# Kernel optimization log

Hardware: AMD Instinct MI355X
Metric: run time of the kernel (lower is better)

Reference implementation:

```python
import jax, jax.numpy as jnp
import numpy as np

BATCH = 4096          # batch_size from init
TEMP = 0.1            # temperature
EPS = 1e-8            # torch CosineSimilarity eps
N = 2 * BATCH


def _neg_flat_idx(bs):
    """Static flat indices of the negative entries of the (N,N) sim matrix:
    everything except the main diagonal and the +-bs diagonals (positives)."""
    n = 2 * bs
    mask = np.ones((n, n), dtype=bool)
    np.fill_diagonal(mask, False)
    r = np.arange(bs)
    mask[r, bs + r] = False
    mask[bs + r, r] = False
    return np.nonzero(mask.reshape(-1))[0]


NEG_IDX = jnp.asarray(_neg_flat_idx(BATCH))  # (N*(N-2),)


def setup_inputs() -> dict:
    key = jax.random.key(0)
    k1, k2 = jax.random.split(key)
    msg = jax.random.normal(k1, (N, 512), dtype=jnp.float32)
    img = jax.random.normal(k2, (N, 512), dtype=jnp.float32)
    return {"msg": msg, "img": img}


def reference(msg, img):
    # cosine similarity via normalized GEMM (norms clamped at eps, per torch)
    mn = msg / jnp.maximum(jnp.linalg.norm(msg, axis=1, keepdims=True), EPS)
    im = img / jnp.maximum(jnp.linalg.norm(img, axis=1, keepdims=True), EPS)
    sim = jnp.matmul(mn, im.T) / TEMP                      # (N, N)

    sim_i_j = jnp.diagonal(sim, offset=BATCH)              # (BATCH,)
    sim_j_i = jnp.diagonal(sim, offset=-BATCH)             # (BATCH,)
    positives = jnp.concatenate([sim_i_j, sim_j_i])[:, None]   # (N, 1)
    negatives = sim.reshape(-1)[NEG_IDX].reshape(N, N - 2)     # (N, N-2)

    logits = jnp.concatenate([positives, negatives], axis=1)   # (N, N-1)
    logp = jax.nn.log_softmax(logits, axis=1)
    # labels are all zero; CrossEntropyLoss(reduction='sum') / N
    loss = -jnp.sum(logp[:, 0]) / N
    acc = jnp.mean((jnp.argmax(logits, axis=1) == 0).astype(jnp.float32))
    return loss, acc
```

## Files before the change

### kernel.cpp

```cpp
#include <hip/hip_runtime.h>
#include <hip/hip_bf16.h>


#define NROWS 8192
#define BATCHD 4096
#define DIM 512
#define BM 128
#define BN 128
#define BK 32
#define NSTEP (DIM / BK)
#define SHIFT 10.0f

typedef short bf16x8 __attribute__((ext_vector_type(8)));
typedef float f32x4 __attribute__((ext_vector_type(4)));

#define GLDS(g, l)                                                             \
    __builtin_amdgcn_global_load_lds(                                          \
        (const __attribute__((address_space(1))) void*)(g),                    \
        (__attribute__((address_space(3))) void*)(l), 16, 0, 0)

__device__ __forceinline__ unsigned f2u_ord(float f) {
    unsigned u = __float_as_uint(f);
    return (u & 0x80000000u) ? ~u : (u | 0x80000000u);
}
__device__ __forceinline__ float u2f_ord(unsigned e) {
    return (e & 0x80000000u) ? __uint_as_float(e & 0x7fffffffu) : __uint_as_float(~e);
}
__device__ __forceinline__ short f2bf(float f) {
    unsigned u = __float_as_uint(f);
    return (short)((u + 0x7fffu + ((u >> 16) & 1u)) >> 16);
}

__global__ __launch_bounds__(64) void normalize_bf16_both(const float* __restrict__ msg,
                                                          const float* __restrict__ img,
                                                          short* __restrict__ mnb,
                                                          short* __restrict__ imb,
                                                          float* __restrict__ rowsum,
                                                          unsigned* __restrict__ rowmax,
                                                          float* __restrict__ accum) {
    if (blockIdx.x < 128) {
        const int i = blockIdx.x * 64 + threadIdx.x;
        rowsum[i] = 0.f;
        rowmax[i] = 0u;
        if (i < 2) accum[i] = 0.f;
    }
    int row = blockIdx.x;
    const float* in;
    short* out;
    float scale;
    if (row < NROWS) { in = msg; out = mnb; scale = 10.0f; }
    else { row -= NROWS; in = img; out = imb; scale = 1.0f; }
    const int lane = threadIdx.x;
    const float* src = in + (size_t)row * DIM + lane * 8;
    float4 v0 = *(const float4*)(src);
    float4 v1 = *(const float4*)(src + 4);
    float ss = v0.x*v0.x + v0.y*v0.y + v0.z*v0.z + v0.w*v0.w
             + v1.x*v1.x + v1.y*v1.y + v1.z*v1.z + v1.w*v1.w;
    #pragma unroll
    for (int off = 1; off < 64; off <<= 1) ss += __shfl_xor(ss, off);
    const float inv = scale / fmaxf(sqrtf(ss), 1e-8f);
    float vv[8] = {v0.x, v0.y, v0.z, v0.w, v1.x, v1.y, v1.z, v1.w};
    bf16x8 o;
    #pragma unroll
    for (int j = 0; j < 8; ++j) o[j] = f2bf(vv[j] * inv);
    *(bf16x8*)(out + (size_t)row * DIM + lane * 8) = o;
}

__global__ __launch_bounds__(256, 4) void simloss_mfma(const short* __restrict__ A,
                                                       const short* __restrict__ B,
                                                       float* __restrict__ rowsum,
                                                       unsigned* __restrict__ rowmax,
                                                       float* __restrict__ rowpos) {
    __shared__ short As[2][BM * BK];
    __shared__ short Bs[2][BN * BK];

    const int tid = threadIdx.x;
    const int lane = tid & 63;
    const int g = lane >> 4;
    const int r16 = lane & 15;
    const int wid = tid >> 6;
    const int wr = wid >> 1;
    const int wc = wid & 1;

    const int bid = blockIdx.x;
    const int xcd = bid & 7;
    const int l = bid >> 3;
    const int by = xcd * 8 + (l & 7);
    const int bx = l >> 3;
    const int rowBase = by * BM;
    const int colBase = bx * BN;

    const int s0 = tid, s1 = tid + 256;
    const int r0 = s0 >> 2, r1 = s1 >> 2;
    const int c0 = (s0 & 3) ^ ((r0 >> 1) & 3);
    const int c1 = (s1 & 3) ^ ((r1 >> 1) & 3);
    const short* gA0 = A + (size_t)(rowBase + r0) * DIM + c0 * 8;
    const short* gA1 = A + (size_t)(rowBase + r1) * DIM + c1 * 8;
    const short* gB0 = B + (size_t)(colBase + r0) * DIM + c0 * 8;
    const short* gB1 = B + (size_t)(colBase + r1) * DIM + c1 * 8;

#define STAGE(b, koff)                                  \
    do {                                                \
        GLDS(gA0 + (koff), &As[b][tid * 8]);            \
        GLDS(gA1 + (koff), &As[b][2048 + tid * 8]);     \
        GLDS(gB0 + (koff), &Bs[b][tid * 8]);            \
        GLDS(gB1 + (koff), &Bs[b][2048 + tid * 8]);     \
    } while (0)

    const int swz = (r16 >> 1) & 3;
    const int aBase = (wr * 64 + r16) * BK + ((g ^ swz) * 8);
    const int bBase = (wc * 64 + r16) * BK + ((g ^ swz) * 8);

    f32x4 acc[4][4] = {};

#define VMCNT(n) asm volatile("s_waitcnt vmcnt(" #n ")" ::: "memory")
#define BAR() __builtin_amdgcn_s_barrier()

    STAGE(0, 0);

    for (int t = 0; t < NSTEP; ++t) {
        const int b = t & 1;
        if (t < NSTEP - 1) {
            STAGE(b ^ 1, (t + 1) * BK);
            VMCNT(4);
        } else {
            VMCNT(0);
        }
        BAR();
        bf16x8 af[4], bfr[4];
        #pragma unroll
        for (int m = 0; m < 4; ++m)
            af[m] = *(const bf16x8*)&As[b][aBase + m * 16 * BK];
        #pragma unroll
        for (int n = 0; n < 4; ++n)
            bfr[n] = *(const bf16x8*)&Bs[b][bBase + n * 16 * BK];
        __builtin_amdgcn_s_setprio(1);
        #pragma unroll
        for (int m = 0; m < 4; ++m)
            #pragma unroll
            for (int n = 0; n < 4; ++n)
                acc[m][n] = __builtin_amdgcn_mfma_f32_16x16x32_bf16(
                    af[m], bfr[n], acc[m][n], 0, 0, 0);
        __builtin_amdgcn_s_setprio(0);
        BAR();
    }

    __syncthreads();
    float* ssum = (float*)&As[0][0];
    float* smx = ssum + 256;
    const int baseRow = rowBase + wr * 64 + g * 4;
    const int baseCol = colBase + wc * 64 + r16;
    #pragma unroll
    for (int m = 0; m < 4; ++m) {
        #pragma unroll
        for (int reg = 0; reg < 4; ++reg) {
            const int i = baseRow + m * 16 + reg;
            const int partner = i ^ BATCHD;
            float sum = 0.f, mx = -1e30f;
            #pragma unroll
            for (int n = 0; n < 4; ++n) {
                const int j = baseCol + n * 16;
                const float s = acc[m][n][reg];
                const bool isDiag = (j == i);
                const bool isPos = (j == partner);
                float e = __expf(s - SHIFT);
                if (isDiag) e = 0.f;
                sum += e;
                if (!isDiag && !isPos) mx = fmaxf(mx, s);
                if (isPos) rowpos[i] = s;
            }
            #pragma unroll
            for (int off = 1; off < 16; off <<= 1) {
                sum += __shfl_xor(sum, off);
                mx = fmaxf(mx, __shfl_xor(mx, off));
            }
            if (r16 == 0) {
                const int rloc = wr * 64 + m * 16 + g * 4 + reg;
                ssum[rloc * 2 + wc] = sum;
                smx[rloc * 2 + wc] = mx;
            }
        }
    }
    __syncthreads();
    if (tid < BM) {
        const float s = ssum[tid * 2 + 0] + ssum[tid * 2 + 1];
        const float mx = fmaxf(smx[tid * 2 + 0], smx[tid * 2 + 1]);
        const int i = rowBase + tid;
        atomicAdd(&rowsum[i], s);
        atomicMax(&rowmax[i], f2u_ord(mx));
    }
#undef STAGE
#undef VMCNT
#undef BAR
}

__global__ __launch_bounds__(256) void finalize_partial(const float* __restrict__ rowsum,
                                                        const unsigned* __restrict__ rowmax,
                                                        const float* __restrict__ rowpos,
                                                        float* __restrict__ accum) {
    const int tid = threadIdx.x;
    const int i = blockIdx.x * 256 + tid;
    const float lse = SHIFT + logf(rowsum[i]);
    const float pos = rowpos[i];
    float lossAcc = lse - pos;
    float hitAcc = (pos >= u2f_ord(rowmax[i])) ? 1.f : 0.f;
    __shared__ float sl[256], sa[256];
    sl[tid] = lossAcc; sa[tid] = hitAcc;
    __syncthreads();
    for (int s = 128; s > 0; s >>= 1) {
        if (tid < s) { sl[tid] += sl[tid + s]; sa[tid] += sa[tid + s]; }
        __syncthreads();
    }
    if (tid == 0) {
        atomicAdd(&accum[0], sl[0]);
        atomicAdd(&accum[1], sa[0]);
    }
}

__global__ void finalize_write(const float* __restrict__ accum, float* __restrict__ out) {
    if (threadIdx.x == 0) {
        out[0] = accum[0] / (float)NROWS;
        out[1] = accum[1] / (float)NROWS;
    }
}

extern "C" void kernel_launch(void* const* d_in, const int* in_sizes, int n_in,
                              void* d_out, int out_size, void* d_ws, size_t ws_size,
                              hipStream_t stream) {
    const float* msg = (const float*)d_in[0];
    const float* img = (const float*)d_in[1];
    float* out = (float*)d_out;

    char* ws = (char*)d_ws;
    const size_t matBytes = (size_t)NROWS * DIM * sizeof(short);
    short* mnb = (short*)ws;
    short* imb = (short*)(ws + matBytes);
    float* rowsum = (float*)(ws + 2 * matBytes);
    unsigned* rowmax = (unsigned*)(ws + 2 * matBytes + NROWS * sizeof(float));
    float* rowpos = (float*)(ws + 2 * matBytes + 2 * NROWS * sizeof(float));
    float* accum = (float*)(ws + 2 * matBytes + 3 * NROWS * sizeof(float));

    normalize_bf16_both<<<2 * NROWS, 64, 0, stream>>>(msg, img, mnb, imb,
                                                      rowsum, rowmax, accum);

    simloss_mfma<<<(NROWS / BM) * (NROWS / BN), 256, 0, stream>>>(mnb, imb, rowsum,
                                                                  rowmax, rowpos);

    finalize_partial<<<NROWS / 256, 256, 0, stream>>>(rowsum, rowmax, rowpos, accum);
    finalize_write<<<1, 64, 0, stream>>>(accum, out);
}
```

Before: 105.7 us.

## Load A fragments directly from global into registers, bypassing LDS

The A operand is no longer staged through shared memory. Each wave loads its A fragments straight from global memory into registers, double-buffered across k-steps with the next step prefetched, while B keeps its LDS double buffer. This cuts LDS footprint and LDS traffic for A and removes the A shared-memory reads. In exchange, A rows shared by the two wave columns are now loaded twice from global/L2, and the loads are uncoalesced 16-byte row-strided accesses that add register pressure.

```diff
diff --git a/kernel.cpp b/kernel.cpp
--- a/kernel.cpp
+++ b/kernel.cpp
@@ -71,7 +71,6 @@
                                                        float* __restrict__ rowsum,
                                                        unsigned* __restrict__ rowmax,
                                                        float* __restrict__ rowpos) {
-    __shared__ short As[2][BM * BK];
     __shared__ short Bs[2][BN * BK];
 
     const int tid = threadIdx.x;
@@ -94,59 +93,63 @@
     const int r0 = s0 >> 2, r1 = s1 >> 2;
     const int c0 = (s0 & 3) ^ ((r0 >> 1) & 3);
     const int c1 = (s1 & 3) ^ ((r1 >> 1) & 3);
-    const short* gA0 = A + (size_t)(rowBase + r0) * DIM + c0 * 8;
-    const short* gA1 = A + (size_t)(rowBase + r1) * DIM + c1 * 8;
     const short* gB0 = B + (size_t)(colBase + r0) * DIM + c0 * 8;
     const short* gB1 = B + (size_t)(colBase + r1) * DIM + c1 * 8;
 
-#define STAGE(b, koff)                                  \
+#define STAGE_B(b, koff)                                \
     do {                                                \
-        GLDS(gA0 + (koff), &As[b][tid * 8]);            \
-        GLDS(gA1 + (koff), &As[b][2048 + tid * 8]);     \
         GLDS(gB0 + (koff), &Bs[b][tid * 8]);            \
         GLDS(gB1 + (koff), &Bs[b][2048 + tid * 8]);     \
     } while (0)
 
+    const short* aP = A + (size_t)(rowBase + wr * 64 + r16) * DIM + g * 8;
+#define LOADA(dst, koff)                                                    \
+    do {                                                                    \
+        _Pragma("unroll") for (int m = 0; m < 4; ++m)                       \
+            dst[m] = *(const bf16x8*)(aP + (size_t)m * 16 * DIM + (koff));  \
+    } while (0)
+
     const int swz = (r16 >> 1) & 3;
-    const int aBase = (wr * 64 + r16) * BK + ((g ^ swz) * 8);
     const int bBase = (wc * 64 + r16) * BK + ((g ^ swz) * 8);
 
     f32x4 acc[4][4] = {};
+    bf16x8 afA[4], afB[4];
 
 #define VMCNT(n) asm volatile("s_waitcnt vmcnt(" #n ")" ::: "memory")
 #define BAR() __builtin_amdgcn_s_barrier()
 
-    STAGE(0, 0);
-
-    for (int t = 0; t < NSTEP; ++t) {
-        const int b = t & 1;
-        if (t < NSTEP - 1) {
-            STAGE(b ^ 1, (t + 1) * BK);
-            VMCNT(4);
-        } else {
-            VMCNT(0);
-        }
-        BAR();
-        bf16x8 af[4], bfr[4];
-        #pragma unroll
-        for (int m = 0; m < 4; ++m)
-            af[m] = *(const bf16x8*)&As[b][aBase + m * 16 * BK];
-        #pragma unroll
-        for (int n = 0; n < 4; ++n)
-            bfr[n] = *(const bf16x8*)&Bs[b][bBase + n * 16 * BK];
-        __builtin_amdgcn_s_setprio(1);
-        #pragma unroll
-        for (int m = 0; m < 4; ++m)
-            #pragma unroll
-            for (int n = 0; n < 4; ++n)
-                acc[m][n] = __builtin_amdgcn_mfma_f32_16x16x32_bf16(
-                    af[m], bfr[n], acc[m][n], 0, 0, 0);
-        __builtin_amdgcn_s_setprio(0);
-        BAR();
+#define STEP(t, b, AF, AFN)                                                  \
+    do {                                                                     \
+        if ((t) < NSTEP - 1) {                                               \
+            STAGE_B((b) ^ 1, ((t) + 1) * BK);                                \
+            LOADA(AFN, ((t) + 1) * BK);                                      \
+            VMCNT(6);                                                        \
+        } else {                                                             \
+            VMCNT(0);                                                        \
+        }                                                                    \
+        BAR();                                                               \
+        bf16x8 bfr[4];                                                       \
+        _Pragma("unroll") for (int n = 0; n < 4; ++n)                        \
+            bfr[n] = *(const bf16x8*)&Bs[b][bBase + n * 16 * BK];            \
+        __builtin_amdgcn_s_setprio(1);                                       \
+        _Pragma("unroll") for (int m = 0; m < 4; ++m)                        \
+            _Pragma("unroll") for (int n = 0; n < 4; ++n)                    \
+                acc[m][n] = __builtin_amdgcn_mfma_f32_16x16x32_bf16(         \
+                    AF[m], bfr[n], acc[m][n], 0, 0, 0);                      \
+        __builtin_amdgcn_s_setprio(0);                                       \
+        BAR();                                                               \
+    } while (0)
+
+    STAGE_B(0, 0);
+    LOADA(afA, 0);
+
+    for (int j = 0; j < NSTEP / 2; ++j) {
+        STEP(2 * j, 0, afA, afB);
+        STEP(2 * j + 1, 1, afB, afA);
     }
 
     __syncthreads();
-    float* ssum = (float*)&As[0][0];
+    float* ssum = (float*)&Bs[0][0];
     float* smx = ssum + 256;
     const int baseRow = rowBase + wr * 64 + g * 4;
     const int baseCol = colBase + wc * 64 + r16;
@@ -189,7 +192,9 @@
         atomicAdd(&rowsum[i], s);
         atomicMax(&rowmax[i], f2u_ord(mx));
     }
-#undef STAGE
+#undef STAGE_B
+#undef LOADA
+#undef STEP
 #undef VMCNT
 #undef BAR
 }
```

Measured after the change: 154.3 us. 1.46x slower.
